# Kernel tuning notes

Measured on AMD Instinct MI355X. Metric: run time of the kernel, lower is better.

The kernel has to match this reference:

```python
import jax, jax.numpy as jnp
import numpy as np

N = 1_000_000          # total nodes
C = 128                # in_channels
NUM_SEGMENTS = 10_000  # number of graphs (= batch.max()+1 in the torch code)


def setup_inputs() -> dict:
    key = jax.random.key(0)
    k1, k2, k3 = jax.random.split(key, 3)
    x = jax.random.normal(k1, (N, C), dtype=jnp.float32)
    batch = jnp.sort(jax.random.randint(k2, (N,), 0, NUM_SEGMENTS, dtype=jnp.int64))
    W = jax.random.normal(k3, (C, 1), dtype=jnp.float32) * (1.0 / np.sqrt(C))
    b = jnp.zeros((1,), dtype=jnp.float32)
    return {"x": x, "batch": batch, "W": W, "b": b}


def reference(x, batch, W, b):
    # attention score: Linear(C->1) followed by Softmax over dim=1 (a size-1
    # axis in the original torch code, so the softmax yields all ones; we
    # faithfully reproduce that math).
    logits = x @ W + b                       # [N, 1]
    score = jax.nn.softmax(logits, axis=1)   # [N, 1] (== ones)
    weighted = score * x                     # [N, C]
    # scatter_add keyed by batch -> per-graph sum
    out = jax.ops.segment_sum(weighted, batch, num_segments=NUM_SEGMENTS)  # [G, C]
    return out
```

## Files before the change

### kernel.cpp

```cpp
#include <hip/hip_runtime.h>


#define C 128
#define ROWS_PER_WAVE 64
#define WAVES_PER_BLOCK 4
#define BLOCK_THREADS (WAVES_PER_BLOCK * 64)
#define UNROLL 8

typedef float f4 __attribute__((ext_vector_type(4)));

__device__ __forceinline__ void flush_acc(float* __restrict__ out, int seg,
                                          int col4, f4& acc) {
    float* o = out + (size_t)seg * C + 4 * col4;
    atomicAdd(o + 0, acc.x);
    atomicAdd(o + 1, acc.y);
    atomicAdd(o + 2, acc.z);
    atomicAdd(o + 3, acc.w);
    acc = (f4){0.f, 0.f, 0.f, 0.f};
}

__global__ __launch_bounds__(BLOCK_THREADS)
void segsum_kernel(const f4* __restrict__ xv,
                   const int* __restrict__ batch,
                   float* __restrict__ out,
                   int n_rows, int n_segs) {
    const int wave = blockIdx.x * WAVES_PER_BLOCK + (threadIdx.x >> 6);
    const int lane = threadIdx.x & 63;
    const int half = lane >> 5;
    const int col4 = lane & 31;

    long row0 = (long)wave * ROWS_PER_WAVE;
    if (row0 >= n_rows) return;
    long row_end = row0 + ROWS_PER_WAVE;
    if (row_end > n_rows) row_end = n_rows;
    const int nrows_w = (int)(row_end - row0);

    long bidx = row0 + lane;
    if (bidx > (long)n_rows - 1) bidx = (long)n_rows - 1;
    int bval = batch[bidx];
    bval = min(max(bval, 0), n_segs - 1);

    f4 acc = (f4){0.f, 0.f, 0.f, 0.f};
    int cur = __shfl(bval, half);

    const f4* base = xv + row0 * (C / 4) + col4;

    int i = 0;
    for (; i + 2 * UNROLL <= nrows_w; i += 2 * UNROLL) {
        f4 v[UNROLL];
#pragma unroll
        for (int j = 0; j < UNROLL; ++j)
            v[j] = __builtin_nontemporal_load(base + (long)(i + 2 * j + half) * (C / 4));
#pragma unroll
        for (int j = 0; j < UNROLL; ++j) {
            int seg = __shfl(bval, i + 2 * j + half);
            if (seg != cur) {
                flush_acc(out, cur, col4, acc);
                cur = seg;
            }
            acc += v[j];
        }
    }
    for (; i + 1 < nrows_w; i += 2) {
        f4 v = __builtin_nontemporal_load(base + (long)(i + half) * (C / 4));
        int seg = __shfl(bval, i + half);
        if (seg != cur) {
            flush_acc(out, cur, col4, acc);
            cur = seg;
        }
        acc += v;
    }
    if (i < nrows_w) {
        int seg = __shfl(bval, i);
        if (half == 0) {
            f4 v = __builtin_nontemporal_load(base + (long)i * (C / 4));
            if (seg != cur) {
                flush_acc(out, cur, col4, acc);
                cur = seg;
            }
            acc += v;
        }
    }
    flush_acc(out, cur, col4, acc);
}

extern "C" void kernel_launch(void* const* d_in, const int* in_sizes, int n_in,
                              void* d_out, int out_size, void* d_ws, size_t ws_size,
                              hipStream_t stream) {
    const float* x     = (const float*)d_in[0];
    const int*   batch = (const int*)d_in[1];
    float* out = (float*)d_out;

    const int n_rows = in_sizes[0] / C;
    const int n_segs = out_size / C;

    hipMemsetAsync(d_out, 0, (size_t)out_size * sizeof(float), stream);

    const int n_waves  = (n_rows + ROWS_PER_WAVE - 1) / ROWS_PER_WAVE;
    const int n_blocks = (n_waves + WAVES_PER_BLOCK - 1) / WAVES_PER_BLOCK;

    segsum_kernel<<<n_blocks, BLOCK_THREADS, 0, stream>>>(
        (const f4*)x, batch, out, n_rows, n_segs);
}
```

Baseline: 657.6 us.

## Assign one wave per segment via binary search, drop atomics and memset

Replaces the row-chunked scheme with one wave per output segment. Each wave binary-searches the sorted batch array for its row range, sums its rows with no segment-change checks, combines the two halves with a shuffle, and writes its output row directly. This removes all atomic adds and the output memset. It adds two binary searches per wave, leaves load balance dependent on segment sizes (about 100 rows each here), and relies on batch being sorted.

```diff
diff --git a/kernel.cpp b/kernel.cpp
--- a/kernel.cpp
+++ b/kernel.cpp
@@ -2,86 +2,60 @@
 
 
 #define C 128
-#define ROWS_PER_WAVE 64
 #define WAVES_PER_BLOCK 4
 #define BLOCK_THREADS (WAVES_PER_BLOCK * 64)
 #define UNROLL 8
 
 typedef float f4 __attribute__((ext_vector_type(4)));
 
-__device__ __forceinline__ void flush_acc(float* __restrict__ out, int seg,
-                                          int col4, f4& acc) {
-    float* o = out + (size_t)seg * C + 4 * col4;
-    atomicAdd(o + 0, acc.x);
-    atomicAdd(o + 1, acc.y);
-    atomicAdd(o + 2, acc.z);
-    atomicAdd(o + 3, acc.w);
-    acc = (f4){0.f, 0.f, 0.f, 0.f};
-}
-
 __global__ __launch_bounds__(BLOCK_THREADS)
 void segsum_kernel(const f4* __restrict__ xv,
                    const int* __restrict__ batch,
                    float* __restrict__ out,
                    int n_rows, int n_segs) {
-    const int wave = blockIdx.x * WAVES_PER_BLOCK + (threadIdx.x >> 6);
+    const int g = blockIdx.x * WAVES_PER_BLOCK + (threadIdx.x >> 6);
+    if (g >= n_segs) return;
     const int lane = threadIdx.x & 63;
     const int half = lane >> 5;
     const int col4 = lane & 31;
 
-    long row0 = (long)wave * ROWS_PER_WAVE;
-    if (row0 >= n_rows) return;
-    long row_end = row0 + ROWS_PER_WAVE;
-    if (row_end > n_rows) row_end = n_rows;
-    const int nrows_w = (int)(row_end - row0);
-
-    long bidx = row0 + lane;
-    if (bidx > (long)n_rows - 1) bidx = (long)n_rows - 1;
-    int bval = batch[bidx];
-    bval = min(max(bval, 0), n_segs - 1);
+    int s;
+    {
+        int lo = 0, hi = n_rows;
+        while (lo < hi) { int m = (lo + hi) >> 1; if (batch[m] < g) lo = m + 1; else hi = m; }
+        s = lo;
+    }
+    int e;
+    {
+        int lo = s, hi = n_rows;
+        while (lo < hi) { int m = (lo + hi) >> 1; if (batch[m] <= g) lo = m + 1; else hi = m; }
+        e = lo;
+    }
 
     f4 acc = (f4){0.f, 0.f, 0.f, 0.f};
-    int cur = __shfl(bval, half);
-
-    const f4* base = xv + row0 * (C / 4) + col4;
+    const f4* base = xv + (long)s * (C / 4) + col4;
+    const int nr = e - s;
 
     int i = 0;
-    for (; i + 2 * UNROLL <= nrows_w; i += 2 * UNROLL) {
+    for (; i + 2 * UNROLL <= nr; i += 2 * UNROLL) {
         f4 v[UNROLL];
 #pragma unroll
         for (int j = 0; j < UNROLL; ++j)
             v[j] = __builtin_nontemporal_load(base + (long)(i + 2 * j + half) * (C / 4));
 #pragma unroll
-        for (int j = 0; j < UNROLL; ++j) {
-            int seg = __shfl(bval, i + 2 * j + half);
-            if (seg != cur) {
-                flush_acc(out, cur, col4, acc);
-                cur = seg;
-            }
+        for (int j = 0; j < UNROLL; ++j)
             acc += v[j];
-        }
     }
-    for (; i + 1 < nrows_w; i += 2) {
-        f4 v = __builtin_nontemporal_load(base + (long)(i + half) * (C / 4));
-        int seg = __shfl(bval, i + half);
-        if (seg != cur) {
-            flush_acc(out, cur, col4, acc);
-            cur = seg;
-        }
-        acc += v;
-    }
-    if (i < nrows_w) {
-        int seg = __shfl(bval, i);
-        if (half == 0) {
-            f4 v = __builtin_nontemporal_load(base + (long)i * (C / 4));
-            if (seg != cur) {
-                flush_acc(out, cur, col4, acc);
-                cur = seg;
-            }
-            acc += v;
-        }
-    }
-    flush_acc(out, cur, col4, acc);
+    for (; i + 1 < nr; i += 2)
+        acc += __builtin_nontemporal_load(base + (long)(i + half) * (C / 4));
+    if (i < nr && half == 0)
+        acc += __builtin_nontemporal_load(base + (long)i * (C / 4));
+
+#pragma unroll
+    for (int k = 0; k < 4; ++k)
+        acc[k] += __shfl_xor(acc[k], 32);
+    if (half == 0)
+        *(f4*)(out + (size_t)g * C + 4 * col4) = acc;
 }
 
 extern "C" void kernel_launch(void* const* d_in, const int* in_sizes, int n_in,
@@ -94,10 +68,8 @@
     const int n_rows = in_sizes[0] / C;
     const int n_segs = out_size / C;
 
-    hipMemsetAsync(d_out, 0, (size_t)out_size * sizeof(float), stream);
 
-    const int n_waves  = (n_rows + ROWS_PER_WAVE - 1) / ROWS_PER_WAVE;
-    const int n_blocks = (n_waves + WAVES_PER_BLOCK - 1) / WAVES_PER_BLOCK;
+    const int n_blocks = (n_segs + WAVES_PER_BLOCK - 1) / WAVES_PER_BLOCK;
 
     segsum_kernel<<<n_blocks, BLOCK_THREADS, 0, stream>>>(
         (const f4*)x, batch, out, n_rows, n_segs);
```

Result: faster. 639.1 us (-2.8%).
